# Optimization experiments

Hardware: AMD Instinct MI355X
Metric: run time of the kernel (lower is better)

The kernel has to match this reference:

```python
import jax, jax.numpy as jnp
import numpy as np

B, N, E, H = 4, 4096, 1024, 16
D = E // H            # head_dim = 64
P_DIM = 64            # proj_dim; feature dim = 2*P_DIM = 128
EPS = 1e-4


def setup_inputs() -> dict:
    key = jax.random.key(0)
    ks = jax.random.split(key, 9)
    x = jax.random.normal(ks[0], (B, N, E), jnp.float32)
    init = 0.02
    Wq = jax.random.normal(ks[1], (E, E), jnp.float32) * init
    Wk = jax.random.normal(ks[2], (E, E), jnp.float32) * init
    Wv = jax.random.normal(ks[3], (E, E), jnp.float32) * init
    Wo = jax.random.normal(ks[4], (E, E), jnp.float32) * init
    bq = jnp.zeros((E,), jnp.float32)
    bk = jnp.zeros((E,), jnp.float32)
    bv = jnp.zeros((E,), jnp.float32)
    bo = jnp.zeros((E,), jnp.float32)
    # orthogonal random projection matrix (proj_dim, head_dim), fixed (non-trainable)
    g = np.random.default_rng(0).normal(size=(P_DIM, D))
    P = jnp.asarray(np.linalg.qr(g)[0], jnp.float32)
    return dict(x=x, Wq=Wq, bq=bq, Wk=Wk, bk=bk, Wv=Wv, bv=bv, Wo=Wo, bo=bo, P=P)


def _heads(z):
    # (B, N, E) -> (B, H, N, D)
    return z.reshape(B, N, H, D).transpose(0, 2, 1, 3)


def _normalize(z):
    return z / (jnp.linalg.norm(z, axis=-1, keepdims=True) + EPS)


def reference(x, Wq, bq, Wk, bk, Wv, bv, Wo, bo, P):
    q = _heads(x @ Wq.T + bq)
    k = _heads(x @ Wk.T + bk)
    v = _heads(x @ Wv.T + bv)
    q = _normalize(q)
    k = _normalize(k)
    scale = H ** 0.25
    qp = jnp.einsum('bhnd,ed->bhne', q, P) * scale
    kp = jnp.einsum('bhnd,ed->bhne', k, P) * scale
    fscale = P_DIM ** (-0.5)   # x.shape[-1]**-0.5 with last dim = proj_dim
    qf = jnp.concatenate([jnp.sin(qp), jnp.cos(qp)], axis=-1) * fscale  # (B,H,N,2p)
    kf = jnp.concatenate([jnp.sin(kp), jnp.cos(kp)], axis=-1) * fscale
    # non-causal linear attention: q @ (k^T v)
    kv = jnp.einsum('bhme,bhmd->bhed', kf, v)          # (B,H,2p,D)
    o = jnp.einsum('bhne,bhed->bhnd', qf, kv)          # (B,H,N,D)
    o = o.transpose(0, 2, 1, 3).reshape(B, N, E)
    return o @ Wo.T + bo
```

## Files before the change

### kernel.cpp

```cpp
#include <hip/hip_runtime.h>
#include <hip/hip_bf16.h>
#include <stdint.h>


typedef __bf16 bf16x8 __attribute__((ext_vector_type(8)));
typedef float f32x4 __attribute__((ext_vector_type(4)));

#define AS1 __attribute__((address_space(1)))
#define AS3 __attribute__((address_space(3)))

__device__ __forceinline__ void gl2lds16(const void* g, void* l) {
    __builtin_amdgcn_global_load_lds((const AS1 void*)g, (AS3 void*)l, 16, 0, 0);
}

#define CFENCE asm volatile("" ::: "memory")

static constexpr int GM = 16384, GN = 1024, GK = 1024;
static constexpr int KV_SLABS = 8;

__global__ void detect_kernel(const unsigned short* __restrict__ x,
                              int* __restrict__ flag) {
    __shared__ int s;
    const int lane = threadIdx.x;
    if (lane == 0) s = 0;
    __syncthreads();
    int cnt = 0;
#pragma unroll
    for (int i = 0; i < 2; ++i) {
        const unsigned short u = x[i * 64 + lane];
        const int e = (u >> 7) & 0xFF;
        cnt += (e >= 117 && e <= 131) ? 1 : 0;
    }
    atomicAdd(&s, cnt);
    __syncthreads();
    if (lane == 0) *flag = (s >= 100) ? 1 : 0;
}

__global__ __launch_bounds__(256) void cvt_kernel(
    const void* __restrict__ src, __hip_bfloat16* __restrict__ dst,
    int n, const int* __restrict__ flag) {
    if (*flag) return;
    const int i = (blockIdx.x * 256 + threadIdx.x) * 8;
    if (i >= n) return;
    const float* s = (const float*)src + i;
    const float4 a = *(const float4*)s;
    const float4 b = *(const float4*)(s + 4);
    union { uint4 u; __hip_bfloat16 h[8]; } pk;
    pk.h[0] = __float2bfloat16(a.x); pk.h[1] = __float2bfloat16(a.y);
    pk.h[2] = __float2bfloat16(a.z); pk.h[3] = __float2bfloat16(a.w);
    pk.h[4] = __float2bfloat16(b.x); pk.h[5] = __float2bfloat16(b.y);
    pk.h[6] = __float2bfloat16(b.z); pk.h[7] = __float2bfloat16(b.w);
    *(uint4*)(dst + i) = pk.u;
}

__global__ __launch_bounds__(512, 2) void gemm256_kernel(
    const void* __restrict__ Adirect,
    const __hip_bfloat16* __restrict__ Acvt,
    const void* __restrict__ Wr, const __hip_bfloat16* __restrict__ Wc,
    const void* __restrict__ bias_raw,
    void* __restrict__ Cout,
    const int* __restrict__ flag, int last)
{
    __shared__ unsigned short smem[65536];

    const int tid  = threadIdx.x;
    const int lane = tid & 63;
    const int w    = tid >> 6;
    const int wm   = w >> 2, wn = w & 3;
    const int lr   = lane & 15, lk = lane >> 4;

    const int id  = blockIdx.x;
    const int xcd = id & 7;
    const int s   = id >> 3;
    const int m0  = (xcd * 8 + (s >> 2)) * 256;
    const int n0  = (s & 3) * 256;
    const int fl  = *flag;

    const __hip_bfloat16* A = fl ? (const __hip_bfloat16*)Adirect : Acvt;
    const __hip_bfloat16* W = fl ? (const __hip_bfloat16*)Wr : Wc;
    const __hip_bfloat16* Ab = A + (size_t)m0 * GK;
    const __hip_bfloat16* Wb = W + (size_t)n0 * GK;

    f32x4 acc[8][4];
#pragma unroll
    for (int i = 0; i < 8; ++i)
#pragma unroll
        for (int j = 0; j < 4; ++j)
            acc[i][j] = (f32x4){0.f, 0.f, 0.f, 0.f};

    const int jj8 = (lk ^ ((lr >> 1) & 3)) * 8;
    int offA[8], offB[4];
#pragma unroll
    for (int i = 0; i < 8; ++i)
        offA[i] = (wm * 128 + i * 16 + lr) * 32 + jj8;
#pragma unroll
    for (int j = 0; j < 4; ++j)
        offB[j] = 8192 + (wn * 64 + j * 16 + lr) * 32 + jj8;

    size_t gofs[2];
    int    ldso[2];
#pragma unroll
    for (int p = 0; p < 2; ++p) {
        const int chunk = p * 512 + tid;
        const int row   = chunk >> 2, c = chunk & 3;
        const int cs    = c ^ ((row >> 1) & 3);
        gofs[p] = (size_t)row * GK + cs * 8;
        ldso[p] = (p * 512 + w * 64) * 16;
    }

    auto stage2 = [&](int t, int part) {
        char* base = (char*)smem + (t & 3) * 32768 + ldso[part];
        const size_t go = gofs[part] + (size_t)(t * 32);
        gl2lds16(Ab + go, base);
        gl2lds16(Wb + go, base + 16384);
    };

    stage2(0, 0); stage2(0, 1);
    stage2(1, 0); stage2(1, 1);
    stage2(2, 0); stage2(2, 1);
    asm volatile("s_waitcnt vmcnt(8)" ::: "memory");
    __builtin_amdgcn_s_barrier();

    auto tile = [&](int slot, int t, bool do_stage, int gate) {
        const unsigned short* sl = smem + slot * 16384;
        bf16x8 af[4], bfr[4], af2[4];
#pragma unroll
        for (int i = 0; i < 4; ++i) af[i] = *(const bf16x8*)&sl[offA[i]];
#pragma unroll
        for (int j = 0; j < 4; ++j) bfr[j] = *(const bf16x8*)&sl[offB[j]];
        if (do_stage) stage2(t + 3, 0);
        CFENCE;
        __builtin_amdgcn_s_barrier();
        __builtin_amdgcn_s_setprio(1);
#pragma unroll
        for (int i = 0; i < 4; ++i)
#pragma unroll
            for (int j = 0; j < 4; ++j)
                acc[i][j] = __builtin_amdgcn_mfma_f32_16x16x32_bf16(
                    af[i], bfr[j], acc[i][j], 0, 0, 0);
        __builtin_amdgcn_s_setprio(0);
        CFENCE;
        __builtin_amdgcn_s_barrier();
#pragma unroll
        for (int i = 0; i < 4; ++i) af2[i] = *(const bf16x8*)&sl[offA[4 + i]];
        if (do_stage) stage2(t + 3, 1);
        if (gate == 8)      asm volatile("s_waitcnt vmcnt(8)" ::: "memory");
        else if (gate == 4) asm volatile("s_waitcnt vmcnt(4)" ::: "memory");
        else                asm volatile("s_waitcnt vmcnt(0)" ::: "memory");
        __builtin_amdgcn_s_barrier();
        __builtin_amdgcn_s_setprio(1);
#pragma unroll
        for (int i = 0; i < 4; ++i)
#pragma unroll
            for (int j = 0; j < 4; ++j)
                acc[4 + i][j] = __builtin_amdgcn_mfma_f32_16x16x32_bf16(
                    af2[i], bfr[j], acc[4 + i][j], 0, 0, 0);
        __builtin_amdgcn_s_setprio(0);
        CFENCE;
        __builtin_amdgcn_s_barrier();
    };

#pragma unroll 1
    for (int t = 0; t < 28; t += 4) {
        tile(0, t + 0, true, 8);
        tile(1, t + 1, true, 8);
        tile(2, t + 2, true, 8);
        tile(3, t + 3, true, 8);
    }
    tile(0, 28, true, 8);
    tile(1, 29, false, 4);
    tile(2, 30, false, 0);
    tile(3, 31, false, 0);

    const bool f32out = (last != 0) && (fl == 0);
    if (f32out) {
#pragma unroll
        for (int j = 0; j < 4; ++j) {
            const int col = n0 + wn * 64 + j * 16 + lr;
            const float bv = ((const float*)bias_raw)[col];
#pragma unroll
            for (int i = 0; i < 8; ++i) {
                const int rbase = m0 + wm * 128 + i * 16 + lk * 4;
#pragma unroll
                for (int r = 0; r < 4; ++r)
                    ((float*)Cout)[(size_t)(rbase + r) * GN + col] =
                        acc[i][j][r] + bv;
            }
        }
        return;
    }

    unsigned short* sC = smem;
#pragma unroll
    for (int j = 0; j < 4; ++j) {
        const int col = wn * 64 + j * 16 + lr;
        const float bv = fl ? __bfloat162float(((const __hip_bfloat16*)bias_raw)[n0 + col])
                            : ((const float*)bias_raw)[n0 + col];
        const int c_hi = col >> 3, off = col & 7;
#pragma unroll
        for (int i = 0; i < 8; ++i) {
            const int rb = wm * 128 + i * 16 + lk * 4;
#pragma unroll
            for (int r = 0; r < 4; ++r) {
                const int row = rb + r;
                const int phys = c_hi ^ (row & 7);
                __hip_bfloat16 hv = __float2bfloat16(acc[i][j][r] + bv);
                sC[row * 256 + phys * 8 + off] = *(unsigned short*)&hv;
            }
        }
    }
    __syncthreads();
    {
        const int row = tid >> 1, half = tid & 1;
        __hip_bfloat16* dst = (__hip_bfloat16*)Cout +
            (size_t)(m0 + row) * GN + n0 + half * 128;
#pragma unroll
        for (int q = 0; q < 16; ++q) {
            const int chunk = half * 16 + q;
            const int phys  = chunk ^ (row & 7);
            *(uint4*)(dst + q * 8) = *(const uint4*)&sC[row * 256 + phys * 8];
        }
    }
}

__device__ __forceinline__ void load_P(const void* Praw, int f,
                                       __hip_bfloat16* sP, int tid) {
    const int e = tid >> 2, q = tid & 3;
    union { uint4 u[2]; __hip_bfloat16 h[16]; } pk;
    if (f) {
        pk.u[0] = *(const uint4*)((const __hip_bfloat16*)Praw + e * 64 + q * 16);
        pk.u[1] = *(const uint4*)((const __hip_bfloat16*)Praw + e * 64 + q * 16 + 8);
    } else {
        const float* ps = (const float*)Praw + e * 64 + q * 16;
#pragma unroll
        for (int j = 0; j < 16; ++j) pk.h[j] = __float2bfloat16(ps[j]);
    }
    *(uint4*)&sP[e * 72 + q * 16]     = pk.u[0];
    *(uint4*)&sP[e * 72 + q * 16 + 8] = pk.u[1];
}

__device__ __forceinline__ float sumsq16(uint4 a, uint4 b) {
    union { uint4 u; __hip_bfloat16 h[8]; } x0, x1;
    x0.u = a; x1.u = b;
    float ss = 0.f;
#pragma unroll
    for (int j = 0; j < 8; ++j) {
        float v0 = __bfloat162float(x0.h[j]); ss += v0 * v0;
        float v1 = __bfloat162float(x1.h[j]); ss += v1 * v1;
    }
    return ss;
}

__global__ __launch_bounds__(256) void kv_kernel(
    const __hip_bfloat16* __restrict__ Km,
    const __hip_bfloat16* __restrict__ Vm,
    const void* __restrict__ Praw,
    float* __restrict__ PKV,
    const int* __restrict__ flag)
{
    __shared__ __hip_bfloat16 sK[64 * 72];
    __shared__ __hip_bfloat16 sVT[64 * 72];
    __shared__ __hip_bfloat16 sP[64 * 72];
    __shared__ __hip_bfloat16 sKFT[128 * 72];
    __shared__ float sRN[64];

    const int tid  = threadIdx.x;
    const int lane = tid & 63;
    const int w    = tid >> 6;
    const int lr   = lane & 15, lk = lane >> 4;
    const int bh   = blockIdx.y;
    const int b    = bh >> 4, h = bh & 15;
    const int nst  = blockIdx.x * 512;
    const int f    = *flag;
    const int n    = tid >> 2, q2 = tid & 3;

    load_P(Praw, f, sP, tid);

    f32x4 acck[2][4];
#pragma unroll
    for (int i = 0; i < 2; ++i)
#pragma unroll
        for (int j = 0; j < 4; ++j)
            acck[i][j] = (f32x4){0.f, 0.f, 0.f, 0.f};

    size_t base = ((size_t)(b * 4096 + nst + n)) * 1024 + h * 64 + q2 * 16;
    uint4 ka = *(const uint4*)(Km + base), kb = *(const uint4*)(Km + base + 8);
    uint4 va = *(const uint4*)(Vm + base), vb = *(const uint4*)(Vm + base + 8);

    for (int s = 0; s < 8; ++s) {
        __syncthreads();
        *(uint4*)&sK[n * 72 + q2 * 16]     = ka;
        *(uint4*)&sK[n * 72 + q2 * 16 + 8] = kb;
        {
            union { uint4 u[2]; __hip_bfloat16 h[16]; } vv;
            vv.u[0] = va; vv.u[1] = vb;
#pragma unroll
            for (int j = 0; j < 16; ++j) sVT[(q2 * 16 + j) * 72 + n] = vv.h[j];
        }
        {
            float ss = sumsq16(ka, kb);
            ss += __shfl_xor(ss, 1, 64);
            ss += __shfl_xor(ss, 2, 64);
            if (q2 == 0) sRN[n] = 2.0f / (sqrtf(ss) + 1e-4f);
        }
        if (s < 7) {
            base = ((size_t)(b * 4096 + nst + (s + 1) * 64 + n)) * 1024 + h * 64 + q2 * 16;
            ka = *(const uint4*)(Km + base); kb = *(const uint4*)(Km + base + 8);
            va = *(const uint4*)(Vm + base); vb = *(const uint4*)(Vm + base + 8);
        }
        {
            bf16x8 afr0 = *(const bf16x8*)&sK[(w * 16 + lr) * 72 + lk * 8];
            bf16x8 afr1 = *(const bf16x8*)&sK[(w * 16 + lr) * 72 + 32 + lk * 8];
            float rn[4];
#pragma unroll
            for (int r = 0; r < 4; ++r) rn[r] = sRN[w * 16 + lk * 4 + r];
#pragma unroll
            for (int eb = 0; eb < 4; ++eb) {
                f32x4 pa = (f32x4){0.f, 0.f, 0.f, 0.f};
                bf16x8 b0 = *(const bf16x8*)&sP[(eb * 16 + lr) * 72 + lk * 8];
                bf16x8 b1 = *(const bf16x8*)&sP[(eb * 16 + lr) * 72 + 32 + lk * 8];
                pa = __builtin_amdgcn_mfma_f32_16x16x32_bf16(afr0, b0, pa, 0, 0, 0);
                pa = __builtin_amdgcn_mfma_f32_16x16x32_bf16(afr1, b1, pa, 0, 0, 0);
                const int col = eb * 16 + lr;
#pragma unroll
                for (int r = 0; r < 4; ++r) {
                    const int row = w * 16 + lk * 4 + r;
                    float sv, cv;
                    __sincosf(pa[r] * rn[r], &sv, &cv);
                    sKFT[col * 72 + row]        = __float2bfloat16(sv * 0.125f);
                    sKFT[(col + 64) * 72 + row] = __float2bfloat16(cv * 0.125f);
                }
            }
        }
        __syncthreads();
#pragma unroll
        for (int ks = 0; ks < 2; ++ks) {
            bf16x8 a2[2], b2[4];
            a2[0] = *(const bf16x8*)&sKFT[(w * 16 + lr) * 72 + ks * 32 + lk * 8];
            a2[1] = *(const bf16x8*)&sKFT[((w + 4) * 16 + lr) * 72 + ks * 32 + lk * 8];
#pragma unroll
            for (int db = 0; db < 4; ++db)
                b2[db] = *(const bf16x8*)&sVT[(db * 16 + lr) * 72 + ks * 32 + lk * 8];
#pragma unroll
            for (int i = 0; i < 2; ++i)
#pragma unroll
                for (int db = 0; db < 4; ++db)
                    acck[i][db] = __builtin_amdgcn_mfma_f32_16x16x32_bf16(
                        a2[i], b2[db], acck[i][db], 0, 0, 0);
        }
    }

    float* out = PKV + ((size_t)blockIdx.x * 64 + bh) * 8192;
#pragma unroll
    for (int i = 0; i < 2; ++i)
#pragma unroll
        for (int db = 0; db < 4; ++db)
#pragma unroll
            for (int r = 0; r < 4; ++r) {
                const int e = (w + 4 * i) * 16 + lk * 4 + r;
                const int d = db * 16 + lr;
                out[e * 64 + d] = acck[i][db][r];
            }
}

__global__ __launch_bounds__(256) void kv_reduce_kernel(
    const float* __restrict__ PKV, float* __restrict__ gKV)
{
    const int i = (blockIdx.x * 256 + threadIdx.x) * 4;
    f32x4 s = (f32x4){0.f, 0.f, 0.f, 0.f};
#pragma unroll
    for (int sl = 0; sl < KV_SLABS; ++sl) {
        const float4 v = *(const float4*)(PKV + (size_t)sl * 64 * 8192 + i);
        s[0] += v.x; s[1] += v.y; s[2] += v.z; s[3] += v.w;
    }
    *(float4*)(gKV + i) = *(float4*)&s;
}

__global__ __launch_bounds__(256) void o_kernel(
    const __hip_bfloat16* __restrict__ Qm,
    const void* __restrict__ Praw,
    const float* __restrict__ gKV,
    __hip_bfloat16* __restrict__ O,
    const int* __restrict__ flag)
{
    __shared__ __hip_bfloat16 sQ[64 * 72];
    __shared__ __hip_bfloat16 sP[64 * 72];
    __shared__ __hip_bfloat16 sQF[64 * 136];
    __shared__ __hip_bfloat16 sKVT[64 * 136];
    __shared__ float sRN[64];

    const int tid  = threadIdx.x;
    const int lane = tid & 63;
    const int w    = tid >> 6;
    const int lr   = lane & 15, lk = lane >> 4;
    const int bh   = blockIdx.y;
    const int b    = bh >> 4, h = bh & 15;
    const int nst  = blockIdx.x * 256;
    const int f    = *flag;
    const int n    = tid >> 2, q2 = tid & 3;

    load_P(Praw, f, sP, tid);
    {
        const float* kvsrc = gKV + (size_t)bh * 8192;
        for (int t = tid; t < 8192; t += 256) {
            const int e = t >> 6, d = t & 63;
            sKVT[d * 136 + e] = __float2bfloat16(kvsrc[t]);
        }
    }

    size_t base = ((size_t)(b * 4096 + nst + n)) * 1024 + h * 64 + q2 * 16;
    uint4 qa = *(const uint4*)(Qm + base), qb = *(const uint4*)(Qm + base + 8);

    __syncthreads();

    for (int s = 0; s < 4; ++s) {
        const int gn0 = nst + s * 64;
        *(uint4*)&sQ[n * 72 + q2 * 16]     = qa;
        *(uint4*)&sQ[n * 72 + q2 * 16 + 8] = qb;
        {
            float ss = sumsq16(qa, qb);
            ss += __shfl_xor(ss, 1, 64);
            ss += __shfl_xor(ss, 2, 64);
            if (q2 == 0) sRN[n] = 2.0f / (sqrtf(ss) + 1e-4f);
        }
        if (s < 3) {
            base = ((size_t)(b * 4096 + nst + (s + 1) * 64 + n)) * 1024 + h * 64 + q2 * 16;
            qa = *(const uint4*)(Qm + base); qb = *(const uint4*)(Qm + base + 8);
        }
        {
            bf16x8 afr0 = *(const bf16x8*)&sQ[(w * 16 + lr) * 72 + lk * 8];
            bf16x8 afr1 = *(const bf16x8*)&sQ[(w * 16 + lr) * 72 + 32 + lk * 8];
            float rn[4];
#pragma unroll
            for (int r = 0; r < 4; ++r) rn[r] = sRN[w * 16 + lk * 4 + r];
#pragma unroll
            for (int eb = 0; eb < 4; ++eb) {
                f32x4 pa = (f32x4){0.f, 0.f, 0.f, 0.f};
                bf16x8 b0 = *(const bf16x8*)&sP[(eb * 16 + lr) * 72 + lk * 8];
                bf16x8 b1 = *(const bf16x8*)&sP[(eb * 16 + lr) * 72 + 32 + lk * 8];
                pa = __builtin_amdgcn_mfma_f32_16x16x32_bf16(afr0, b0, pa, 0, 0, 0);
                pa = __builtin_amdgcn_mfma_f32_16x16x32_bf16(afr1, b1, pa, 0, 0, 0);
                const int col = eb * 16 + lr;
#pragma unroll
                for (int r = 0; r < 4; ++r) {
                    const int row = w * 16 + lk * 4 + r;
                    float sv, cv;
                    __sincosf(pa[r] * rn[r], &sv, &cv);
                    sQF[row * 136 + col]      = __float2bfloat16(sv * 0.125f);
                    sQF[row * 136 + 64 + col] = __float2bfloat16(cv * 0.125f);
                }
            }
        }
        f32x4 oacc[4];
#pragma unroll
        for (int nb = 0; nb < 4; ++nb) oacc[nb] = (f32x4){0.f, 0.f, 0.f, 0.f};
#pragma unroll
        for (int ks = 0; ks < 4; ++ks) {
            bf16x8 aa = *(const bf16x8*)&sQF[(w * 16 + lr) * 136 + ks * 32 + lk * 8];
#pragma unroll
            for (int nb = 0; nb < 4; ++nb) {
                bf16x8 bb = *(const bf16x8*)&sKVT[(nb * 16 + lr) * 136 + ks * 32 + lk * 8];
                oacc[nb] = __builtin_amdgcn_mfma_f32_16x16x32_bf16(aa, bb, oacc[nb], 0, 0, 0);
            }
        }
#pragma unroll
        for (int nb = 0; nb < 4; ++nb)
#pragma unroll
            for (int r = 0; r < 4; ++r)
                sQ[(w * 16 + lk * 4 + r) * 72 + nb * 16 + lr] =
                    __float2bfloat16(oacc[nb][r]);
        {
            uint4 o0 = *(uint4*)&sQ[n * 72 + q2 * 16];
            uint4 o1 = *(uint4*)&sQ[n * 72 + q2 * 16 + 8];
            const size_t obase = ((size_t)(b * 4096 + gn0 + n)) * 1024 + h * 64 + q2 * 16;
            *(uint4*)(O + obase)     = o0;
            *(uint4*)(O + obase + 8) = o1;
        }
    }
}

extern "C" void kernel_launch(void* const* d_in, const int* in_sizes, int n_in,
                              void* d_out, int out_size, void* d_ws, size_t ws_size,
                              hipStream_t stream)
{
    (void)in_sizes; (void)n_in; (void)out_size; (void)ws_size;
    const void* x  = d_in[0];
    const void* Wq = d_in[1];
    const void* bq = d_in[2];
    const void* Wk = d_in[3];
    const void* bk = d_in[4];
    const void* Wv = d_in[5];
    const void* bv = d_in[6];
    const void* Wo = d_in[7];
    const void* bo = d_in[8];
    const void* P  = d_in[9];

    constexpr size_t XE = (size_t)GM * GN;
    constexpr size_t WE = (size_t)GN * GK;
    constexpr size_t KVE = (size_t)64 * 128 * 64;

    __hip_bfloat16* xb  = (__hip_bfloat16*)d_ws;
    __hip_bfloat16* wqb = xb + XE;
    __hip_bfloat16* wkb = wqb + WE;
    __hip_bfloat16* wvb = wkb + WE;
    __hip_bfloat16* wob = wvb + WE;
    __hip_bfloat16* R1  = wob + WE;
    __hip_bfloat16* R2  = R1 + XE;
    float* gKV = (float*)(R2 + XE);
    float* PKV = gKV + KVE;
    int* flag  = (int*)(PKV + (size_t)KV_SLABS * 64 * 8192);

    dim3 blk(256);
    hipLaunchKernelGGL(detect_kernel, dim3(1), dim3(64), 0, stream,
                       (const unsigned short*)x, flag);

    hipLaunchKernelGGL(cvt_kernel, dim3(8192), blk, 0, stream, x,  xb,  (int)XE, flag);
    hipLaunchKernelGGL(cvt_kernel, dim3(512),  blk, 0, stream, Wq, wqb, (int)WE, flag);
    hipLaunchKernelGGL(cvt_kernel, dim3(512),  blk, 0, stream, Wk, wkb, (int)WE, flag);
    hipLaunchKernelGGL(cvt_kernel, dim3(512),  blk, 0, stream, Wv, wvb, (int)WE, flag);
    hipLaunchKernelGGL(cvt_kernel, dim3(512),  blk, 0, stream, Wo, wob, (int)WE, flag);

    hipLaunchKernelGGL(gemm256_kernel, dim3(256), dim3(512), 0, stream,
                       x, xb, Wk, wkb, bk, R1, flag, 0);
    hipLaunchKernelGGL(gemm256_kernel, dim3(256), dim3(512), 0, stream,
                       x, xb, Wv, wvb, bv, R2, flag, 0);
    hipLaunchKernelGGL(kv_kernel, dim3(KV_SLABS, 64), blk, 0, stream, R1, R2, P, PKV, flag);
    hipLaunchKernelGGL(kv_reduce_kernel, dim3(512), blk, 0, stream, PKV, gKV);
    hipLaunchKernelGGL(gemm256_kernel, dim3(256), dim3(512), 0, stream,
                       x, xb, Wq, wqb, bq, R2, flag, 0);
    hipLaunchKernelGGL(o_kernel, dim3(16, 64), blk, 0, stream, R2, P, gKV, R1, flag);
    hipLaunchKernelGGL(gemm256_kernel, dim3(256), dim3(512), 0, stream,
                       R1, R1, Wo, wob, bo, d_out, flag, 1);
}
```

Measured before the change: 371.2 us.

## Fuse K and V projection GEMMs sharing A tiles; batch weight conversions

Replaces the two separate K and V projection GEMMs with one kernel that loads each A tile once and multiplies it by both weight tiles, producing two outputs. It also merges the four weight fp32->bf16 conversions into a single launch. The aim is to halve the reads of x for K/V and cut launch overhead. The trade-offs are a new kernel with 128x128 tiles and no double buffering, in place of the tuned 256-tile GEMM, and higher register pressure from two accumulator sets.

```diff
diff --git a/kernel.cpp b/kernel.cpp
--- a/kernel.cpp
+++ b/kernel.cpp
@@ -36,13 +36,7 @@
     if (lane == 0) *flag = (s >= 100) ? 1 : 0;
 }
 
-__global__ __launch_bounds__(256) void cvt_kernel(
-    const void* __restrict__ src, __hip_bfloat16* __restrict__ dst,
-    int n, const int* __restrict__ flag) {
-    if (*flag) return;
-    const int i = (blockIdx.x * 256 + threadIdx.x) * 8;
-    if (i >= n) return;
-    const float* s = (const float*)src + i;
+__device__ __forceinline__ void cvt8(const float* s, __hip_bfloat16* d) {
     const float4 a = *(const float4*)s;
     const float4 b = *(const float4*)(s + 4);
     union { uint4 u; __hip_bfloat16 h[8]; } pk;
@@ -50,7 +44,152 @@
     pk.h[2] = __float2bfloat16(a.z); pk.h[3] = __float2bfloat16(a.w);
     pk.h[4] = __float2bfloat16(b.x); pk.h[5] = __float2bfloat16(b.y);
     pk.h[6] = __float2bfloat16(b.z); pk.h[7] = __float2bfloat16(b.w);
-    *(uint4*)(dst + i) = pk.u;
+    *(uint4*)d = pk.u;
+}
+
+__global__ __launch_bounds__(256) void cvt_kernel(
+    const void* __restrict__ src, __hip_bfloat16* __restrict__ dst,
+    int n, const int* __restrict__ flag) {
+    if (*flag) return;
+    const int i = (blockIdx.x * 256 + threadIdx.x) * 8;
+    if (i >= n) return;
+    cvt8((const float*)src + i, dst + i);
+}
+
+__global__ __launch_bounds__(256) void cvt4_kernel(
+    const void* __restrict__ s0, __hip_bfloat16* __restrict__ d0,
+    const void* __restrict__ s1, __hip_bfloat16* __restrict__ d1,
+    const void* __restrict__ s2, __hip_bfloat16* __restrict__ d2,
+    const void* __restrict__ s3, __hip_bfloat16* __restrict__ d3,
+    const int* __restrict__ flag) {
+    if (*flag) return;
+    const int which = blockIdx.x >> 9;
+    const int i = ((blockIdx.x & 511) * 256 + threadIdx.x) * 8;
+    const float* s = (const float*)(which == 0 ? s0 : which == 1 ? s1
+                                   : which == 2 ? s2 : s3) + i;
+    __hip_bfloat16* d = (which == 0 ? d0 : which == 1 ? d1
+                         : which == 2 ? d2 : d3) + i;
+    cvt8(s, d);
+}
+
+__global__ __launch_bounds__(256, 2) void gemm2_kernel(
+    const void* __restrict__ Adirect,
+    const __hip_bfloat16* __restrict__ Acvt,
+    const void* __restrict__ W0r, const __hip_bfloat16* __restrict__ W0c,
+    const void* __restrict__ W1r, const __hip_bfloat16* __restrict__ W1c,
+    const void* __restrict__ b0r, const void* __restrict__ b1r,
+    void* __restrict__ o0, void* __restrict__ o1,
+    const int* __restrict__ flag)
+{
+    __shared__ unsigned short smem[3 * 128 * 64];
+    unsigned short* sA  = smem;
+    unsigned short* sB0 = smem + 128 * 64;
+    unsigned short* sB1 = smem + 2 * 128 * 64;
+
+    const int tid  = threadIdx.x;
+    const int lane = tid & 63;
+    const int w    = tid >> 6;
+    const int wm   = w >> 1, wn = w & 1;
+    const int lr   = lane & 15, lk = lane >> 4;
+
+    const int id    = blockIdx.x;
+    const int xcd   = id & 7;
+    const int slot  = id >> 3;
+    const int m0    = (xcd * 16 + (slot & 15)) * 128;
+    const int n0    = (slot >> 4) * 128;
+    const int fl    = *flag;
+
+    const __hip_bfloat16* A  = fl ? (const __hip_bfloat16*)Adirect : Acvt;
+    const __hip_bfloat16* W0 = fl ? (const __hip_bfloat16*)W0r : W0c;
+    const __hip_bfloat16* W1 = fl ? (const __hip_bfloat16*)W1r : W1c;
+
+    f32x4 acc[2][4][4];
+#pragma unroll
+    for (int t = 0; t < 2; ++t)
+#pragma unroll
+        for (int i = 0; i < 4; ++i)
+#pragma unroll
+            for (int j = 0; j < 4; ++j)
+                acc[t][i][j] = (f32x4){0.f, 0.f, 0.f, 0.f};
+
+    const __hip_bfloat16* Ab  = A + (size_t)m0 * GK;
+    const __hip_bfloat16* W0b = W0 + (size_t)n0 * GK;
+    const __hip_bfloat16* W1b = W1 + (size_t)n0 * GK;
+
+    for (int k0 = 0; k0 < GK; k0 += 64) {
+#pragma unroll
+        for (int j = 0; j < 4; ++j) {
+            const int chunk = j * 256 + tid;
+            const int row   = chunk >> 3;
+            const int c     = chunk & 7;
+            const int cs    = c ^ (row & 7);
+            const size_t go = (size_t)row * GK + k0 + cs * 8;
+            const int lo = (j * 256 + w * 64) * 16;
+            gl2lds16(Ab  + go, (char*)sA  + lo);
+            gl2lds16(W0b + go, (char*)sB0 + lo);
+            gl2lds16(W1b + go, (char*)sB1 + lo);
+        }
+        __syncthreads();
+#pragma unroll
+        for (int kk = 0; kk < 64; kk += 32) {
+            const int jj = ((kk >> 3) + lk) ^ (lr & 7);
+            bf16x8 af[4], b0f[4], b1f[4];
+#pragma unroll
+            for (int i = 0; i < 4; ++i)
+                af[i] = *(const bf16x8*)&sA[(wm * 64 + i * 16 + lr) * 64 + jj * 8];
+#pragma unroll
+            for (int j = 0; j < 4; ++j)
+                b0f[j] = *(const bf16x8*)&sB0[(wn * 64 + j * 16 + lr) * 64 + jj * 8];
+#pragma unroll
+            for (int j = 0; j < 4; ++j)
+                b1f[j] = *(const bf16x8*)&sB1[(wn * 64 + j * 16 + lr) * 64 + jj * 8];
+#pragma unroll
+            for (int i = 0; i < 4; ++i)
+#pragma unroll
+                for (int j = 0; j < 4; ++j) {
+                    acc[0][i][j] = __builtin_amdgcn_mfma_f32_16x16x32_bf16(
+                        af[i], b0f[j], acc[0][i][j], 0, 0, 0);
+                    acc[1][i][j] = __builtin_amdgcn_mfma_f32_16x16x32_bf16(
+                        af[i], b1f[j], acc[1][i][j], 0, 0, 0);
+                }
+        }
+        __syncthreads();
+    }
+
+    __hip_bfloat16* sC = (__hip_bfloat16*)smem;
+#pragma unroll
+    for (int t = 0; t < 2; ++t) {
+        const void* bias_raw = t ? b1r : b0r;
+        void* Cout = t ? o1 : o0;
+#pragma unroll
+        for (int j = 0; j < 4; ++j) {
+            const int col = wn * 64 + j * 16 + lr;
+            const float bv = fl ? __bfloat162float(((const __hip_bfloat16*)bias_raw)[n0 + col])
+                                : ((const float*)bias_raw)[n0 + col];
+            const int c2 = col >> 3, o = col & 7;
+#pragma unroll
+            for (int i = 0; i < 4; ++i) {
+                const int rb = wm * 64 + i * 16 + lk * 4;
+#pragma unroll
+                for (int r = 0; r < 4; ++r) {
+                    const int row = rb + r;
+                    sC[row * 128 + (c2 ^ (row & 7)) * 8 + o] =
+                        __float2bfloat16(acc[t][i][j][r] + bv);
+                }
+            }
+        }
+        __syncthreads();
+        {
+            const int row = tid >> 1, hf = tid & 1;
+            __hip_bfloat16* dst = (__hip_bfloat16*)Cout + (size_t)(m0 + row) * GN + n0 + hf * 64;
+#pragma unroll
+            for (int q = 0; q < 8; ++q) {
+                const int cc = (hf * 8 + q) ^ (row & 7);
+                *(uint4*)(dst + q * 8) = *(const uint4*)&sC[row * 128 + cc * 8];
+            }
+        }
+        __syncthreads();
+    }
 }
 
 __global__ __launch_bounds__(512, 2) void gemm256_kernel(
@@ -514,16 +653,12 @@
     hipLaunchKernelGGL(detect_kernel, dim3(1), dim3(64), 0, stream,
                        (const unsigned short*)x, flag);
 
-    hipLaunchKernelGGL(cvt_kernel, dim3(8192), blk, 0, stream, x,  xb,  (int)XE, flag);
-    hipLaunchKernelGGL(cvt_kernel, dim3(512),  blk, 0, stream, Wq, wqb, (int)WE, flag);
-    hipLaunchKernelGGL(cvt_kernel, dim3(512),  blk, 0, stream, Wk, wkb, (int)WE, flag);
-    hipLaunchKernelGGL(cvt_kernel, dim3(512),  blk, 0, stream, Wv, wvb, (int)WE, flag);
-    hipLaunchKernelGGL(cvt_kernel, dim3(512),  blk, 0, stream, Wo, wob, (int)WE, flag);
-
-    hipLaunchKernelGGL(gemm256_kernel, dim3(256), dim3(512), 0, stream,
-                       x, xb, Wk, wkb, bk, R1, flag, 0);
-    hipLaunchKernelGGL(gemm256_kernel, dim3(256), dim3(512), 0, stream,
-                       x, xb, Wv, wvb, bv, R2, flag, 0);
+    hipLaunchKernelGGL(cvt_kernel, dim3(8192), blk, 0, stream, x, xb, (int)XE, flag);
+    hipLaunchKernelGGL(cvt4_kernel, dim3(2048), blk, 0, stream,
+                       Wq, wqb, Wk, wkb, Wv, wvb, Wo, wob, flag);
+
+    hipLaunchKernelGGL(gemm2_kernel, dim3(1024), blk, 0, stream,
+                       x, xb, Wk, wkb, Wv, wvb, bk, bv, R1, R2, flag);
     hipLaunchKernelGGL(kv_kernel, dim3(KV_SLABS, 64), blk, 0, stream, R1, R2, P, PKV, flag);
     hipLaunchKernelGGL(kv_reduce_kernel, dim3(512), blk, 0, stream, PKV, gKV);
     hipLaunchKernelGGL(gemm256_kernel, dim3(256), dim3(512), 0, stream,
```

After: 364.4 us. Within noise of the previous version (-1.8%).
